# Optimization experiments

Measured on AMD Instinct MI355X. Metric: run time of the kernel, lower is better.

## Reference

```python
import jax, jax.numpy as jnp
import numpy as np

IM_SIZE = (256, 256)
OVERSAMP = 1.25
WIDTH = 6
BETA = float(np.pi * np.sqrt((WIDTH / OVERSAMP * (OVERSAMP - 0.5)) ** 2 - 0.8))
OS_SIZE = tuple(int(np.ceil(OVERSAMP * n)) for n in IM_SIZE)  # (320, 320)
D = 2


def _kb(x):
    # Kaiser-Bessel interpolation kernel: i0(beta*sqrt(1-x^2)) for |x|<=1 (sigpy convention)
    return jnp.i0(BETA * jnp.sqrt(jnp.maximum(1.0 - x * x, 0.0)))


def setup_inputs() -> dict:
    key = jax.random.key(0)
    k1, k2, k3 = jax.random.split(key, 3)
    N, C = 1, 8
    img_r = jax.random.normal(k1, (N, C) + IM_SIZE, dtype=jnp.float32)
    img_i = jax.random.normal(k2, (N, C) + IM_SIZE, dtype=jnp.float32)
    # trajectory in [-N_i/2, N_i/2] per the class docstring
    trj = (jax.random.uniform(k3, (N, 64, 4096, D), dtype=jnp.float32) - 0.5) * 256.0
    return {"img_r": img_r, "img_i": img_i, "trj": trj}


def _nufft_forward(img_r, img_i, trj):
    img = (img_r + 1j * img_i).astype(jnp.complex64)  # (N, C, H, W)
    nd = img.ndim
    # --- apodization (inverse FT of KB kernel), separable per axis ---
    for a in range(D):
        n, osn = IM_SIZE[a], OS_SIZE[a]
        idx = jnp.arange(n, dtype=jnp.float32)
        arg = jnp.sqrt(BETA ** 2 - (np.pi * WIDTH * (idx - n // 2) / osn) ** 2)
        apod = arg / jnp.sinh(arg)
        shape = [1] * nd
        shape[nd - D + a] = n
        img = img * apod.reshape(shape)
    # --- scale + centered zero-pad to oversampled grid ---
    img = img / np.sqrt(float(np.prod(IM_SIZE)))
    pads = [(0, 0)] * (nd - D) + [(((o - n) // 2), (o - n) - ((o - n) // 2))
                                  for n, o in zip(IM_SIZE, OS_SIZE)]
    img = jnp.pad(img, pads)
    # --- centered FFT (ifftshift -> fftn(norm=None) -> fftshift) ---
    axes = tuple(range(-D, 0))
    ksp_os = jnp.fft.fftshift(jnp.fft.fftn(jnp.fft.ifftshift(img, axes=axes), axes=axes), axes=axes)
    # --- scale trajectory to oversampled grid coordinates ---
    scale = jnp.array([OS_SIZE[a] / IM_SIZE[a] for a in range(D)], jnp.float32)
    shift = jnp.array([OS_SIZE[a] // 2 for a in range(D)], jnp.float32)
    coord = trj * scale + shift  # (N, R, S, 2)
    x0 = jnp.ceil(coord - WIDTH / 2.0)
    # --- KB interpolation: fixed 6x6 neighbor loop, vectorized gather over all points ---
    N = img.shape[0]
    out = jnp.zeros((N,) + img.shape[1:nd - D] + coord.shape[1:-1], jnp.complex64)

    def gather(grid, ix, iy):  # grid (C, Hos, Wos), ix/iy (R, S) -> (C, R, S)
        return grid[:, ix, iy]

    for dx in range(WIDTH):
        px = x0[..., 0] + dx
        wx = _kb((px - coord[..., 0]) / (WIDTH / 2.0))
        ix = px.astype(jnp.int32) % OS_SIZE[0]
        for dy in range(WIDTH):
            py = x0[..., 1] + dy
            wy = _kb((py - coord[..., 1]) / (WIDTH / 2.0))
            iy = py.astype(jnp.int32) % OS_SIZE[1]
            vals = jax.vmap(gather)(ksp_os, ix, iy)  # (N, C, R, S)
            out = out + vals * (wx * wy)[:, None, :, :]
    return out / (WIDTH ** D)


def reference(img_r, img_i, trj):
    return _nufft_forward(img_r, img_i, trj)
```

## Files before the change

### kernel.cpp

```cpp
#include <hip/hip_runtime.h>
#include <math.h>

#define NCH   8
#define IMN   256
#define OSN   320
#define NPTS  (64*4096)
#define KD    512
#define BETA_F   10.9551078f
#define BETA2_F  120.014389f
#define APOD_C   0.05890486225f
#define GROWS 326
#define GCOLS 328
#define GPITCH (GCOLS * NCH)

typedef unsigned short u16;
typedef unsigned int   u32;
typedef __attribute__((ext_vector_type(8))) short s16x8;
typedef __attribute__((ext_vector_type(4))) float f32x4;
typedef __attribute__((ext_vector_type(2))) float f32x2;

__device__ __forceinline__ u32 f2bf(float f) {
    u32 u = __float_as_uint(f);
    return (u + 0x7FFFu + ((u >> 16) & 1u)) >> 16;
}

__device__ __forceinline__ float i0f(float t) {
    if (t < 3.75f) {
        float y = t * t * (1.0f / 14.0625f);
        return 1.0f + y * (3.5156229f + y * (3.0899424f + y * (1.2067492f +
                     y * (0.2659732f + y * (0.0360768f + y * 0.0045813f)))));
    }
    float z = 3.75f / t;
    float p = 0.39894228f + z * (0.01328592f + z * (0.00225319f + z * (-0.00157565f +
              z * (0.00916281f + z * (-0.02057706f + z * (0.02635537f +
              z * (-0.01647633f + z * 0.00392377f)))))));
    return expf(t) * rsqrtf(t) * p;
}

__device__ __forceinline__ float apodf(int i) {
    float x = APOD_C * (float)(i - IMN / 2);
    float arg = sqrtf(BETA2_F - x * x);
    float e = expf(arg);
    float sh = 0.5f * (e - 1.0f / e);
    return arg / sh;
}

__global__ void prep(const float* __restrict__ r, const float* __restrict__ im,
                     u32* __restrict__ B1, u32* __restrict__ B2,
                     u32* __restrict__ A) {
    const int b = blockIdx.x, t = threadIdx.x;
    if (b < (OSN * IMN) / 256) {
        int idx = b * 256 + t;
        int k = idx >> 8, j = idx & 255;
        int p = (k * (j + 32)) % OSN;
        float th = (2.0f * (float)M_PI / (float)OSN) * (float)p;
        float s = ((k + j) & 1) ? -1.0f : 1.0f;
        float sn, cs;
        sincosf(th, &sn, &cs);
        float re = s * cs, imv = -s * sn;
        B1[idx] = f2bf(re) | (f2bf(-imv) << 16);
        B2[idx] = f2bf(imv) | (f2bf(re) << 16);
    } else {
        int idx = (b - (OSN * IMN) / 256) * 256 + t;
        int i2 = idx & 255, i1 = (idx >> 8) & 255;
        float w = apodf(i1) * apodf(i2) * (1.0f / 256.0f);
        A[idx] = f2bf(r[idx] * w) | (f2bf(im[idx] * w) << 16);
    }
}

__launch_bounds__(64)
__global__ void gemm1(const short* __restrict__ Abf, const short* __restrict__ B1,
                      const short* __restrict__ B2, short* __restrict__ Tb) {
    const int c = blockIdx.z;
    const int mBase = blockIdx.y * 32;
    const int nBase = blockIdx.x * 32;
    const int t = threadIdx.x;
    const int fm = t & 15, fq = (t >> 4) * 8;
    const short* pa0  = Abf + (long)(c * IMN + mBase + fm) * KD + fq;
    const short* pa1  = pa0 + 16 * KD;
    const short* pb10 = B1 + (long)(nBase + fm) * KD + fq;
    const short* pb11 = pb10 + 16 * KD;
    const short* pb20 = B2 + (long)(nBase + fm) * KD + fq;
    const short* pb21 = pb20 + 16 * KD;
    f32x4 zz = {0.f, 0.f, 0.f, 0.f};
    f32x4 accRe[2][2], accIm[2][2];
    #pragma unroll
    for (int i = 0; i < 2; i++)
        #pragma unroll
        for (int j = 0; j < 2; j++) { accRe[i][j] = zz; accIm[i][j] = zz; }

    #pragma unroll
    for (int kc = 0; kc < 16; kc++) {
        const int kb = kc * 32;
        s16x8 a0  = *(const s16x8*)(pa0  + kb);
        s16x8 a1  = *(const s16x8*)(pa1  + kb);
        s16x8 b10 = *(const s16x8*)(pb10 + kb);
        s16x8 b11 = *(const s16x8*)(pb11 + kb);
        s16x8 b20 = *(const s16x8*)(pb20 + kb);
        s16x8 b21 = *(const s16x8*)(pb21 + kb);
        accRe[0][0] = __builtin_amdgcn_mfma_f32_16x16x32_bf16(a0, b10, accRe[0][0], 0, 0, 0);
        accRe[0][1] = __builtin_amdgcn_mfma_f32_16x16x32_bf16(a0, b11, accRe[0][1], 0, 0, 0);
        accRe[1][0] = __builtin_amdgcn_mfma_f32_16x16x32_bf16(a1, b10, accRe[1][0], 0, 0, 0);
        accRe[1][1] = __builtin_amdgcn_mfma_f32_16x16x32_bf16(a1, b11, accRe[1][1], 0, 0, 0);
        accIm[0][0] = __builtin_amdgcn_mfma_f32_16x16x32_bf16(a0, b20, accIm[0][0], 0, 0, 0);
        accIm[0][1] = __builtin_amdgcn_mfma_f32_16x16x32_bf16(a0, b21, accIm[0][1], 0, 0, 0);
        accIm[1][0] = __builtin_amdgcn_mfma_f32_16x16x32_bf16(a1, b20, accIm[1][0], 0, 0, 0);
        accIm[1][1] = __builtin_amdgcn_mfma_f32_16x16x32_bf16(a1, b21, accIm[1][1], 0, 0, 0);
    }
    #pragma unroll
    for (int i = 0; i < 2; i++)
        #pragma unroll
        for (int j = 0; j < 2; j++) {
            int i1b = mBase + i * 16 + (t >> 4) * 4;
            int k2  = nBase + j * 16 + fm;
            s16x8 v;
            #pragma unroll
            for (int r = 0; r < 4; r++) {
                v[2 * r]     = (short)f2bf(accRe[i][j][r]);
                v[2 * r + 1] = (short)f2bf(accIm[i][j][r]);
            }
            *(s16x8*)(Tb + ((long)(c * OSN + k2)) * KD + 2 * i1b) = v;
        }
}

__launch_bounds__(64)
__global__ void gemm2(const short* __restrict__ B1, const short* __restrict__ B2,
                      const short* __restrict__ Tb, u32* __restrict__ Gb) {
    const int c = blockIdx.z;
    const int mBase = blockIdx.y * 32;
    const int nBase = blockIdx.x * 32;
    const int t = threadIdx.x;
    const int fm = t & 15, fq = (t >> 4) * 8;
    const short* pa10 = B1 + (long)(mBase + fm) * KD + fq;
    const short* pa11 = pa10 + 16 * KD;
    const short* pa20 = B2 + (long)(mBase + fm) * KD + fq;
    const short* pa21 = pa20 + 16 * KD;
    const short* pb0  = Tb + ((long)(c * OSN + nBase + fm)) * KD + fq;
    const short* pb1  = pb0 + 16 * KD;
    f32x4 zz = {0.f, 0.f, 0.f, 0.f};
    f32x4 accRe[2][2], accIm[2][2];
    #pragma unroll
    for (int i = 0; i < 2; i++)
        #pragma unroll
        for (int j = 0; j < 2; j++) { accRe[i][j] = zz; accIm[i][j] = zz; }

    #pragma unroll
    for (int kc = 0; kc < 16; kc++) {
        const int kb = kc * 32;
        s16x8 a10 = *(const s16x8*)(pa10 + kb);
        s16x8 a11 = *(const s16x8*)(pa11 + kb);
        s16x8 a20 = *(const s16x8*)(pa20 + kb);
        s16x8 a21 = *(const s16x8*)(pa21 + kb);
        s16x8 b0  = *(const s16x8*)(pb0  + kb);
        s16x8 b1  = *(const s16x8*)(pb1  + kb);
        accRe[0][0] = __builtin_amdgcn_mfma_f32_16x16x32_bf16(a10, b0, accRe[0][0], 0, 0, 0);
        accRe[0][1] = __builtin_amdgcn_mfma_f32_16x16x32_bf16(a10, b1, accRe[0][1], 0, 0, 0);
        accRe[1][0] = __builtin_amdgcn_mfma_f32_16x16x32_bf16(a11, b0, accRe[1][0], 0, 0, 0);
        accRe[1][1] = __builtin_amdgcn_mfma_f32_16x16x32_bf16(a11, b1, accRe[1][1], 0, 0, 0);
        accIm[0][0] = __builtin_amdgcn_mfma_f32_16x16x32_bf16(a20, b0, accIm[0][0], 0, 0, 0);
        accIm[0][1] = __builtin_amdgcn_mfma_f32_16x16x32_bf16(a20, b1, accIm[0][1], 0, 0, 0);
        accIm[1][0] = __builtin_amdgcn_mfma_f32_16x16x32_bf16(a21, b0, accIm[1][0], 0, 0, 0);
        accIm[1][1] = __builtin_amdgcn_mfma_f32_16x16x32_bf16(a21, b1, accIm[1][1], 0, 0, 0);
    }
    #pragma unroll
    for (int i = 0; i < 2; i++)
        #pragma unroll
        for (int j = 0; j < 2; j++) {
            int k2 = nBase + j * 16 + fm;
            int pc  = k2 + 3;
            int pc2 = (k2 < 3) ? (k2 + 323) : ((k2 >= 317) ? (k2 - 317) : -1);
            #pragma unroll
            for (int r = 0; r < 4; r++) {
                int k1 = mBase + i * 16 + (t >> 4) * 4 + r;
                u32 val = f2bf(accRe[i][j][r]) | (f2bf(accIm[i][j][r]) << 16);
                int pr  = k1 + 3;
                int pr2 = (k1 < 3) ? (k1 + 323) : ((k1 >= 317) ? (k1 - 317) : -1);
                Gb[(long)pr * GPITCH + pc * NCH + c] = val;
                if (pr2 >= 0)              Gb[(long)pr2 * GPITCH + pc  * NCH + c] = val;
                if (pc2 >= 0)              Gb[(long)pr  * GPITCH + pc2 * NCH + c] = val;
                if (pr2 >= 0 && pc2 >= 0)  Gb[(long)pr2 * GPITCH + pc2 * NCH + c] = val;
            }
        }
}

__launch_bounds__(256, 4)
__global__ void interp_kernel(const float* __restrict__ trj,
                              const u32* __restrict__ grid,
                              u32* __restrict__ out) {
    const int t = threadIdx.x;
    __shared__ float wxs[64][6], wys[64][6];
    __shared__ int   x0s[64], y0s[64];

    if (t < 128) {
        int ptl = t & 63, axis = t >> 6;
        int pt = blockIdx.x * 64 + ptl;
        float tv = trj[pt * 2 + axis];
        float cc = __fadd_rn(__fmul_rn(tv, 1.25f), 160.0f);
        float v0 = ceilf(__fadd_rn(cc, -3.0f));
        if (axis) y0s[ptl] = (int)v0; else x0s[ptl] = (int)v0;
        float* ws = axis ? wys[ptl] : wxs[ptl];
        #pragma unroll
        for (int d = 0; d < 6; d++) {
            float u = __fdiv_rn(__fsub_rn(v0 + (float)d, cc), 3.0f);
            ws[d] = i0f(BETA_F * sqrtf(fmaxf(1.0f - u * u, 0.0f)));
        }
    }
    __syncthreads();

    const int pl   = t >> 2;
    const int cp4  = (t & 1) * 4;
    const int half = (t >> 1) & 1;
    const int px = x0s[pl] + 3 + half * 3;
    const int py = y0s[pl] + 3;
    const u32* g0 = grid + (long)px * GPITCH + py * NCH + cp4;

    uint4 g[18];
    #pragma unroll
    for (int dx = 0; dx < 3; dx++)
        #pragma unroll
        for (int dy = 0; dy < 6; dy++)
            g[dx * 6 + dy] = *(const uint4*)(g0 + dx * GPITCH + dy * NCH);

    float wx[3], wy[6];
    #pragma unroll
    for (int d = 0; d < 3; d++) wx[d] = wxs[pl][half * 3 + d];
    #pragma unroll
    for (int d = 0; d < 6; d++) wy[d] = wys[pl][d];

    f32x2 a0 = {0.f, 0.f}, a1 = {0.f, 0.f}, a2 = {0.f, 0.f}, a3 = {0.f, 0.f};
    #pragma unroll
    for (int dx = 0; dx < 3; dx++) {
        float wxv = wx[dx];
        #pragma unroll
        for (int dy = 0; dy < 6; dy++) {
            uint4 gv = g[dx * 6 + dy];
            float ww = wxv * wy[dy];
            f32x2 w2 = {ww, ww};
            f32x2 v0v = { __uint_as_float(gv.x << 16), __uint_as_float(gv.x & 0xFFFF0000u) };
            f32x2 v1v = { __uint_as_float(gv.y << 16), __uint_as_float(gv.y & 0xFFFF0000u) };
            f32x2 v2v = { __uint_as_float(gv.z << 16), __uint_as_float(gv.z & 0xFFFF0000u) };
            f32x2 v3v = { __uint_as_float(gv.w << 16), __uint_as_float(gv.w & 0xFFFF0000u) };
            a0 += v0v * w2;
            a1 += v1v * w2;
            a2 += v2v * w2;
            a3 += v3v * w2;
        }
    }
    a0.x += __shfl_xor(a0.x, 2, 64); a0.y += __shfl_xor(a0.y, 2, 64);
    a1.x += __shfl_xor(a1.x, 2, 64); a1.y += __shfl_xor(a1.y, 2, 64);
    a2.x += __shfl_xor(a2.x, 2, 64); a2.y += __shfl_xor(a2.y, 2, 64);
    a3.x += __shfl_xor(a3.x, 2, 64); a3.y += __shfl_xor(a3.y, 2, 64);
    f32x2 sc = {1.0f / 36.0f, 1.0f / 36.0f};
    a0 *= sc; a1 *= sc; a2 *= sc; a3 *= sc;

    __shared__ float2 lds[64][9];
    if (half == 0) {
        lds[pl][cp4]     = make_float2(a0.x, a0.y);
        lds[pl][cp4 + 1] = make_float2(a1.x, a1.y);
        lds[pl][cp4 + 2] = make_float2(a2.x, a2.y);
        lds[pl][cp4 + 3] = make_float2(a3.x, a3.y);
    }
    __syncthreads();
    int c2 = t >> 5, p2 = t & 31;
    float2 va = lds[p2][c2];
    float2 vb = lds[p2 + 32][c2];
    long ob = (long)c2 * NPTS + blockIdx.x * 64;
    out[ob + p2]      = f2bf(va.y) | (f2bf(va.x) << 16);
    out[ob + p2 + 32] = f2bf(vb.y) | (f2bf(vb.x) << 16);
}

extern "C" void kernel_launch(void* const* d_in, const int* in_sizes, int n_in,
                              void* d_out, int out_size, void* d_ws, size_t ws_size,
                              hipStream_t stream) {
    const float* img_r = (const float*)d_in[0];
    const float* img_i = (const float*)d_in[1];
    const float* trj   = (const float*)d_in[2];

    char* ob = (char*)d_out;
    short* Tb  = (short*)(ob);
    u32*  B1u  = (u32*)(ob + 2621440);
    u32*  B2u  = (u32*)(ob + 2949120);
    u32*  Au   = (u32*)(ob + 3276800);
    u32*  Gb   = (u32*)d_ws;

    prep<<<(OSN * IMN) / 256 + (NCH * IMN * IMN) / 256, 256, 0, stream>>>(
        img_r, img_i, B1u, B2u, Au);
    gemm1<<<dim3(OSN / 32, IMN / 32, NCH), 64, 0, stream>>>(
        (const short*)Au, (const short*)B1u, (const short*)B2u, Tb);
    gemm2<<<dim3(OSN / 32, OSN / 32, NCH), 64, 0, stream>>>(
        (const short*)B1u, (const short*)B2u, Tb, Gb);
    interp_kernel<<<NPTS / 64, 256, 0, stream>>>(trj, Gb, (u32*)d_out);
}
```

Before: 117.3 us.

## Derive B2 twiddles in-register and split interp work by channel pairs

```diff
diff --git a/kernel.cpp b/kernel.cpp
--- a/kernel.cpp
+++ b/kernel.cpp
@@ -24,6 +24,17 @@
     return (u + 0x7FFFu + ((u >> 16) & 1u)) >> 16;
 }
 
+__device__ __forceinline__ s16x8 derive_b2(s16x8 b) {
+    union { s16x8 v; u32 d[4]; } in, out;
+    in.v = b;
+    #pragma unroll
+    for (int i = 0; i < 4; i++) {
+        u32 v = in.d[i];
+        out.d[i] = ((v >> 16) | (v << 16)) ^ 0x8000u;
+    }
+    return out.v;
+}
+
 __device__ __forceinline__ float i0f(float t) {
     if (t < 3.75f) {
         float y = t * t * (1.0f / 14.0625f);
@@ -46,8 +57,7 @@
 }
 
 __global__ void prep(const float* __restrict__ r, const float* __restrict__ im,
-                     u32* __restrict__ B1, u32* __restrict__ B2,
-                     u32* __restrict__ A) {
+                     u32* __restrict__ B1, u32* __restrict__ A) {
     const int b = blockIdx.x, t = threadIdx.x;
     if (b < (OSN * IMN) / 256) {
         int idx = b * 256 + t;
@@ -59,7 +69,6 @@
         sincosf(th, &sn, &cs);
         float re = s * cs, imv = -s * sn;
         B1[idx] = f2bf(re) | (f2bf(-imv) << 16);
-        B2[idx] = f2bf(imv) | (f2bf(re) << 16);
     } else {
         int idx = (b - (OSN * IMN) / 256) * 256 + t;
         int i2 = idx & 255, i1 = (idx >> 8) & 255;
@@ -70,7 +79,7 @@
 
 __launch_bounds__(64)
 __global__ void gemm1(const short* __restrict__ Abf, const short* __restrict__ B1,
-                      const short* __restrict__ B2, short* __restrict__ Tb) {
+                      short* __restrict__ Tb) {
     const int c = blockIdx.z;
     const int mBase = blockIdx.y * 32;
     const int nBase = blockIdx.x * 32;
@@ -80,8 +89,6 @@
     const short* pa1  = pa0 + 16 * KD;
     const short* pb10 = B1 + (long)(nBase + fm) * KD + fq;
     const short* pb11 = pb10 + 16 * KD;
-    const short* pb20 = B2 + (long)(nBase + fm) * KD + fq;
-    const short* pb21 = pb20 + 16 * KD;
     f32x4 zz = {0.f, 0.f, 0.f, 0.f};
     f32x4 accRe[2][2], accIm[2][2];
     #pragma unroll
@@ -96,8 +103,8 @@
         s16x8 a1  = *(const s16x8*)(pa1  + kb);
         s16x8 b10 = *(const s16x8*)(pb10 + kb);
         s16x8 b11 = *(const s16x8*)(pb11 + kb);
-        s16x8 b20 = *(const s16x8*)(pb20 + kb);
-        s16x8 b21 = *(const s16x8*)(pb21 + kb);
+        s16x8 b20 = derive_b2(b10);
+        s16x8 b21 = derive_b2(b11);
         accRe[0][0] = __builtin_amdgcn_mfma_f32_16x16x32_bf16(a0, b10, accRe[0][0], 0, 0, 0);
         accRe[0][1] = __builtin_amdgcn_mfma_f32_16x16x32_bf16(a0, b11, accRe[0][1], 0, 0, 0);
         accRe[1][0] = __builtin_amdgcn_mfma_f32_16x16x32_bf16(a1, b10, accRe[1][0], 0, 0, 0);
@@ -124,8 +131,8 @@
 }
 
 __launch_bounds__(64)
-__global__ void gemm2(const short* __restrict__ B1, const short* __restrict__ B2,
-                      const short* __restrict__ Tb, u32* __restrict__ Gb) {
+__global__ void gemm2(const short* __restrict__ B1, const short* __restrict__ Tb,
+                      u32* __restrict__ Gb) {
     const int c = blockIdx.z;
     const int mBase = blockIdx.y * 32;
     const int nBase = blockIdx.x * 32;
@@ -133,8 +140,6 @@
     const int fm = t & 15, fq = (t >> 4) * 8;
     const short* pa10 = B1 + (long)(mBase + fm) * KD + fq;
     const short* pa11 = pa10 + 16 * KD;
-    const short* pa20 = B2 + (long)(mBase + fm) * KD + fq;
-    const short* pa21 = pa20 + 16 * KD;
     const short* pb0  = Tb + ((long)(c * OSN + nBase + fm)) * KD + fq;
     const short* pb1  = pb0 + 16 * KD;
     f32x4 zz = {0.f, 0.f, 0.f, 0.f};
@@ -149,10 +154,10 @@
         const int kb = kc * 32;
         s16x8 a10 = *(const s16x8*)(pa10 + kb);
         s16x8 a11 = *(const s16x8*)(pa11 + kb);
-        s16x8 a20 = *(const s16x8*)(pa20 + kb);
-        s16x8 a21 = *(const s16x8*)(pa21 + kb);
         s16x8 b0  = *(const s16x8*)(pb0  + kb);
         s16x8 b1  = *(const s16x8*)(pb1  + kb);
+        s16x8 a20 = derive_b2(a10);
+        s16x8 a21 = derive_b2(a11);
         accRe[0][0] = __builtin_amdgcn_mfma_f32_16x16x32_bf16(a10, b0, accRe[0][0], 0, 0, 0);
         accRe[0][1] = __builtin_amdgcn_mfma_f32_16x16x32_bf16(a10, b1, accRe[0][1], 0, 0, 0);
         accRe[1][0] = __builtin_amdgcn_mfma_f32_16x16x32_bf16(a11, b0, accRe[1][0], 0, 0, 0);
@@ -207,59 +212,43 @@
     }
     __syncthreads();
 
-    const int pl   = t >> 2;
-    const int cp4  = (t & 1) * 4;
-    const int half = (t >> 1) & 1;
-    const int px = x0s[pl] + 3 + half * 3;
+    const int pl = t >> 2;
+    const int cp = (t & 3) * 2;
+    const int px = x0s[pl] + 3;
     const int py = y0s[pl] + 3;
-    const u32* g0 = grid + (long)px * GPITCH + py * NCH + cp4;
-
-    uint4 g[18];
-    #pragma unroll
-    for (int dx = 0; dx < 3; dx++)
+    const u32* g0 = grid + (long)px * GPITCH + py * NCH + cp;
+
+    uint2 g[36];
+    #pragma unroll
+    for (int dx = 0; dx < 6; dx++)
         #pragma unroll
         for (int dy = 0; dy < 6; dy++)
-            g[dx * 6 + dy] = *(const uint4*)(g0 + dx * GPITCH + dy * NCH);
-
-    float wx[3], wy[6];
-    #pragma unroll
-    for (int d = 0; d < 3; d++) wx[d] = wxs[pl][half * 3 + d];
-    #pragma unroll
-    for (int d = 0; d < 6; d++) wy[d] = wys[pl][d];
-
-    f32x2 a0 = {0.f, 0.f}, a1 = {0.f, 0.f}, a2 = {0.f, 0.f}, a3 = {0.f, 0.f};
-    #pragma unroll
-    for (int dx = 0; dx < 3; dx++) {
+            g[dx * 6 + dy] = *(const uint2*)(g0 + dx * GPITCH + dy * NCH);
+
+    float wx[6], wy[6];
+    #pragma unroll
+    for (int d = 0; d < 6; d++) { wx[d] = wxs[pl][d]; wy[d] = wys[pl][d]; }
+
+    float re0 = 0.f, im0 = 0.f, re1 = 0.f, im1 = 0.f;
+    #pragma unroll
+    for (int dx = 0; dx < 6; dx++) {
         float wxv = wx[dx];
         #pragma unroll
         for (int dy = 0; dy < 6; dy++) {
-            uint4 gv = g[dx * 6 + dy];
+            uint2 gv = g[dx * 6 + dy];
             float ww = wxv * wy[dy];
-            f32x2 w2 = {ww, ww};
-            f32x2 v0v = { __uint_as_float(gv.x << 16), __uint_as_float(gv.x & 0xFFFF0000u) };
-            f32x2 v1v = { __uint_as_float(gv.y << 16), __uint_as_float(gv.y & 0xFFFF0000u) };
-            f32x2 v2v = { __uint_as_float(gv.z << 16), __uint_as_float(gv.z & 0xFFFF0000u) };
-            f32x2 v3v = { __uint_as_float(gv.w << 16), __uint_as_float(gv.w & 0xFFFF0000u) };
-            a0 += v0v * w2;
-            a1 += v1v * w2;
-            a2 += v2v * w2;
-            a3 += v3v * w2;
-        }
-    }
-    a0.x += __shfl_xor(a0.x, 2, 64); a0.y += __shfl_xor(a0.y, 2, 64);
-    a1.x += __shfl_xor(a1.x, 2, 64); a1.y += __shfl_xor(a1.y, 2, 64);
-    a2.x += __shfl_xor(a2.x, 2, 64); a2.y += __shfl_xor(a2.y, 2, 64);
-    a3.x += __shfl_xor(a3.x, 2, 64); a3.y += __shfl_xor(a3.y, 2, 64);
-    f32x2 sc = {1.0f / 36.0f, 1.0f / 36.0f};
-    a0 *= sc; a1 *= sc; a2 *= sc; a3 *= sc;
+            re0 += __uint_as_float(gv.x << 16) * ww;
+            im0 += __uint_as_float(gv.x & 0xFFFF0000u) * ww;
+            re1 += __uint_as_float(gv.y << 16) * ww;
+            im1 += __uint_as_float(gv.y & 0xFFFF0000u) * ww;
+        }
+    }
+    re0 *= (1.0f / 36.0f); im0 *= (1.0f / 36.0f);
+    re1 *= (1.0f / 36.0f); im1 *= (1.0f / 36.0f);
 
     __shared__ float2 lds[64][9];
-    if (half == 0) {
-        lds[pl][cp4]     = make_float2(a0.x, a0.y);
-        lds[pl][cp4 + 1] = make_float2(a1.x, a1.y);
-        lds[pl][cp4 + 2] = make_float2(a2.x, a2.y);
-        lds[pl][cp4 + 3] = make_float2(a3.x, a3.y);
-    }
+    lds[pl][cp]     = make_float2(re0, im0);
+    lds[pl][cp + 1] = make_float2(re1, im1);
     __syncthreads();
     int c2 = t >> 5, p2 = t & 31;
     float2 va = lds[p2][c2];
@@ -279,15 +268,14 @@
     char* ob = (char*)d_out;
     short* Tb  = (short*)(ob);
     u32*  B1u  = (u32*)(ob + 2621440);
-    u32*  B2u  = (u32*)(ob + 2949120);
     u32*  Au   = (u32*)(ob + 3276800);
     u32*  Gb   = (u32*)d_ws;
 
     prep<<<(OSN * IMN) / 256 + (NCH * IMN * IMN) / 256, 256, 0, stream>>>(
-        img_r, img_i, B1u, B2u, Au);
+        img_r, img_i, B1u, Au);
     gemm1<<<dim3(OSN / 32, IMN / 32, NCH), 64, 0, stream>>>(
-        (const short*)Au, (const short*)B1u, (const short*)B2u, Tb);
+        (const short*)Au, (const short*)B1u, Tb);
     gemm2<<<dim3(OSN / 32, OSN / 32, NCH), 64, 0, stream>>>(
-        (const short*)B1u, (const short*)B2u, Tb, Gb);
+        (const short*)B1u, Tb, Gb);
     interp_kernel<<<NPTS / 64, 256, 0, stream>>>(trj, Gb, (u32*)d_out);
 }
```

Measured after the change: 108.3 us. -7.7%, faster.
